# Performance work log

Measured on AMD Instinct MI355X. Metric: run time of the kernel, lower is better.

The kernel has to match this reference:

```python
import jax, jax.numpy as jnp
import numpy as np

DT = 0.01
NJ = 7  # panda: 7 revolute joints, serial chain, fixed base
G_ACC = 9.81


def skew(v):
    x, y, z = v[..., 0], v[..., 1], v[..., 2]
    O = jnp.zeros_like(x)
    return jnp.stack([jnp.stack([O, -z, y], -1),
                      jnp.stack([z, O, -x], -1),
                      jnp.stack([-y, x, O], -1)], -2)


def rodrigues(axis, q):
    # axis [3], q [B] -> [B,3,3]
    K = skew(axis)
    K2 = K @ K
    s = jnp.sin(q)[:, None, None]
    c = jnp.cos(q)[:, None, None]
    return jnp.eye(3, dtype=q.dtype) + s * K + (1.0 - c) * K2


def xmot(E, r, v):
    # motion transform child<-parent; E [B,3,3], r [3], v [B,6] ([w;u] ordering)
    w, u = v[:, :3], v[:, 3:]
    wn = jnp.einsum('bij,bj->bi', E, w)
    un = jnp.einsum('bij,bj->bi', E, u - jnp.cross(jnp.broadcast_to(r, u.shape), w))
    return jnp.concatenate([wn, un], -1)


def crm(v, m):
    # motion cross product v x m
    w, u = v[:, :3], v[:, 3:]
    return jnp.concatenate([jnp.cross(w, m[:, :3]),
                            jnp.cross(w, m[:, 3:]) + jnp.cross(u, m[:, :3])], -1)


def crf(v, f):
    # force cross product v x* f
    w, u = v[:, :3], v[:, 3:]
    n, ff = f[:, :3], f[:, 3:]
    return jnp.concatenate([jnp.cross(w, n) + jnp.cross(u, ff), jnp.cross(w, ff)], -1)


def spatial_inertia(mass, com, inertia):
    # [NJ] / [NJ,3] / [NJ,3,3] -> [NJ,6,6] in [w;v] ordering
    cx = skew(com)
    m = mass[:, None, None]
    top = jnp.concatenate([inertia + m * (cx @ jnp.swapaxes(cx, -1, -2)), m * cx], -1)
    bot = jnp.concatenate([m * jnp.swapaxes(cx, -1, -2),
                           m * jnp.broadcast_to(jnp.eye(3, dtype=mass.dtype), cx.shape)], -1)
    return jnp.concatenate([top, bot], -2)


def aba(q, qd, tau, axes, R_fix, p_fix, mass, com, inertia):
    B = q.shape[0]
    I6 = spatial_inertia(mass, com, inertia)  # [NJ,6,6]
    E_l, S_l, v_l, c_l, IA_l, pA_l = [], [], [], [], [], []
    v_prev = None
    # pass 1: kinematics + bias terms
    for i in range(NJ):
        Rw = jnp.einsum('ij,bjk->bik', R_fix[i], rodrigues(axes[i], q[:, i]))
        E = jnp.swapaxes(Rw, -1, -2)  # parent->child rotation
        S = jnp.concatenate([axes[i], jnp.zeros(3, dtype=q.dtype)])  # [6]
        vJ = qd[:, i:i + 1] * S
        v_i = vJ if i == 0 else xmot(E, p_fix[i], v_prev) + vJ
        c_i = crm(v_i, vJ)
        Iv = jnp.einsum('ij,bj->bi', I6[i], v_i)
        pA_i = crf(v_i, Iv)
        E_l.append(E); S_l.append(S); v_l.append(v_i); c_l.append(c_i)
        IA_l.append(jnp.broadcast_to(I6[i], (B, 6, 6)))
        pA_l.append(pA_i)
        v_prev = v_i
    # pass 2: articulated inertia backward sweep
    U_l = [None] * NJ; d_l = [None] * NJ; uu_l = [None] * NJ
    for i in reversed(range(NJ)):
        S = S_l[i]; IA = IA_l[i]
        U = jnp.einsum('bij,j->bi', IA, S)
        d = jnp.einsum('bi,i->b', U, S)
        uu = tau[:, i] - jnp.einsum('bi,i->b', pA_l[i], S)
        U_l[i], d_l[i], uu_l[i] = U, d, uu
        if i > 0:
            Ia = IA - U[:, :, None] * U[:, None, :] / d[:, None, None]
            pa = pA_l[i] + jnp.einsum('bij,bj->bi', Ia, c_l[i]) + U * (uu / d)[:, None]
            E = E_l[i]; rX = skew(p_fix[i])
            Z = jnp.zeros_like(E)
            Xm = jnp.concatenate([jnp.concatenate([E, Z], -1),
                                  jnp.concatenate([-jnp.einsum('bij,jk->bik', E, rX), E], -1)], -2)
            IA_l[i - 1] = IA_l[i - 1] + jnp.einsum('bji,bjk,bkl->bil', Xm, Ia, Xm)
            fE = jnp.einsum('bji,bj->bi', E, pa[:, 3:])
            nP = jnp.einsum('bji,bj->bi', E, pa[:, :3]) + jnp.cross(jnp.broadcast_to(p_fix[i], fE.shape), fE)
            pA_l[i - 1] = pA_l[i - 1] + jnp.concatenate([nP, fE], -1)
    # pass 3: accelerations (base spatial accel = -gravity)
    a_prev = jnp.broadcast_to(jnp.array([0, 0, 0, 0, 0, G_ACC], dtype=q.dtype), (B, 6))
    qdd = []
    for i in range(NJ):
        ap = xmot(E_l[i], p_fix[i], a_prev) + c_l[i]
        qdd_i = (uu_l[i] - jnp.einsum('bi,bi->b', U_l[i], ap)) / d_l[i]
        a_prev = ap + qdd_i[:, None] * S_l[i]
        qdd.append(qdd_i)
    return jnp.stack(qdd, -1)  # [B,NJ]


def _rx(a):
    c, s = np.cos(a), np.sin(a)
    return np.array([[1, 0, 0], [0, c, -s], [0, s, c]], np.float32)


def setup_inputs() -> dict:
    key = jax.random.key(0)
    k1, k2 = jax.random.split(key)
    B = 262144
    x = 0.5 * jax.random.normal(k1, (B, 2 * NJ), dtype=jnp.float32)
    u = 5.0 * jax.random.normal(k2, (B, NJ), dtype=jnp.float32)
    angles = [0.0, -np.pi / 2, np.pi / 2, np.pi / 2, -np.pi / 2, np.pi / 2, np.pi / 2]
    R_fix = jnp.asarray(np.stack([_rx(a) for a in angles]).astype(np.float32))
    p_fix = jnp.asarray(np.array([[0, 0, 0.333], [0, 0, 0], [0, -0.316, 0], [0.0825, 0, 0],
                                  [-0.0825, 0.384, 0], [0, 0, 0], [0.088, 0, 0]], np.float32))
    axes = jnp.asarray(np.tile(np.array([0, 0, 1], np.float32), (NJ, 1)))
    mass = jnp.asarray(np.array([4.97, 0.65, 3.23, 3.59, 1.23, 1.67, 0.735], np.float32))
    com = jnp.asarray(np.array([[0.003, 0.002, -0.06], [-0.003, -0.028, 0.003], [0.027, 0.039, -0.066],
                                [-0.053, 0.104, 0.027], [-0.012, 0.041, -0.038], [0.06, -0.014, -0.011],
                                [0.01, -0.004, 0.061]], np.float32))
    diags = np.array([[0.7, 0.7, 0.01], [0.008, 0.028, 0.025], [0.037, 0.036, 0.011],
                      [0.026, 0.028, 0.031], [0.036, 0.036, 0.011], [0.002, 0.004, 0.005],
                      [0.012, 0.010, 0.005]], np.float32)
    inertia = jnp.asarray(np.stack([np.diag(v) for v in diags]).astype(np.float32))
    return {"x": x, "u": u, "axes": axes, "R_fix": R_fix, "p_fix": p_fix,
            "mass": mass, "com": com, "inertia": inertia}


def reference(x, u, axes, R_fix, p_fix, mass, com, inertia):
    q, v = x[:, :NJ], x[:, NJ:]
    a = aba(q, v, u, axes, R_fix, p_fix, mass, com, inertia)
    v_next = v + DT * a            # semi-implicit Euler
    q_next = q + DT * v_next
    return jnp.concatenate([q_next, v_next], -1)
```

## Files before the change

### kernel.cpp

```cpp
#include <hip/hip_runtime.h>

#define NJ 7
static constexpr float DT_C    = 0.01f;
static constexpr float G_ACC_C = 9.81f;

static constexpr float RF[NJ][9] = {
    {1,0,0,  0,1,0,  0,0,1},
    {1,0,0,  0,0,1,  0,-1,0},
    {1,0,0,  0,0,-1, 0,1,0},
    {1,0,0,  0,0,-1, 0,1,0},
    {1,0,0,  0,0,1,  0,-1,0},
    {1,0,0,  0,0,-1, 0,1,0},
    {1,0,0,  0,0,-1, 0,1,0},
};
static constexpr float PFX[NJ][3] = {
    {0.f, 0.f, 0.333f},
    {0.f, 0.f, 0.f},
    {0.f, -0.316f, 0.f},
    {0.0825f, 0.f, 0.f},
    {-0.0825f, 0.384f, 0.f},
    {0.f, 0.f, 0.f},
    {0.088f, 0.f, 0.f},
};
static constexpr float MS[NJ] = {4.97f, 0.65f, 3.23f, 3.59f, 1.23f, 1.67f, 0.735f};
static constexpr float CM[NJ][3] = {
    {0.003f, 0.002f, -0.06f},
    {-0.003f, -0.028f, 0.003f},
    {0.027f, 0.039f, -0.066f},
    {-0.053f, 0.104f, 0.027f},
    {-0.012f, 0.041f, -0.038f},
    {0.06f, -0.014f, -0.011f},
    {0.01f, -0.004f, 0.061f},
};
static constexpr float ID[NJ][3] = {
    {0.7f, 0.7f, 0.01f},
    {0.008f, 0.028f, 0.025f},
    {0.037f, 0.036f, 0.011f},
    {0.026f, 0.028f, 0.031f},
    {0.036f, 0.036f, 0.011f},
    {0.002f, 0.004f, 0.005f},
    {0.012f, 0.01f, 0.005f},
};

#define MAKE_E(Rf, s, c)                                                     \
    float E00 = (Rf)[0]*(c) + (Rf)[1]*(s);                                   \
    float E01 = (Rf)[3]*(c) + (Rf)[4]*(s);                                   \
    float E02 = (Rf)[6]*(c) + (Rf)[7]*(s);                                   \
    float E10 = (Rf)[1]*(c) - (Rf)[0]*(s);                                   \
    float E11 = (Rf)[4]*(c) - (Rf)[3]*(s);                                   \
    float E12 = (Rf)[7]*(c) - (Rf)[6]*(s);                                   \
    float E20 = (Rf)[2];                                                     \
    float E21 = (Rf)[5];                                                     \
    float E22 = (Rf)[8];

extern "C" __global__ __launch_bounds__(256)
void aba_step_kernel(const float* __restrict__ x, const float* __restrict__ u,
                     float* __restrict__ out, int B)
{
    int b = blockIdx.x * blockDim.x + threadIdx.x;
    if (b >= B) return;
    const int xb = b * (2*NJ);

    float cl0[NJ], cl1[NJ], cl3[NJ], cl4[NJ];
    float pA[NJ][6];

    {
        float v0=0.f, v1=0.f, v2=0.f, v3=0.f, v4=0.f, v5=0.f;
        #pragma unroll
        for (int i = 0; i < NJ; ++i) {
            float qi = x[xb + i];
            float qd = x[xb + NJ + i];
            float s, c;
            __sincosf(qi, &s, &c);
            MAKE_E(RF[i], s, c)
            if (i == 0) {
                v0 = 0.f; v1 = 0.f; v2 = qd; v3 = 0.f; v4 = 0.f; v5 = 0.f;
            } else {
                const float px = PFX[i][0], py = PFX[i][1], pz = PFX[i][2];
                float t0 = v3 - (py*v2 - pz*v1);
                float t1 = v4 - (pz*v0 - px*v2);
                float t2 = v5 - (px*v1 - py*v0);
                float nw0 = E00*v0 + E01*v1 + E02*v2;
                float nw1 = E10*v0 + E11*v1 + E12*v2;
                float nw2 = E20*v0 + E21*v1 + E22*v2;
                float nu0 = E00*t0 + E01*t1 + E02*t2;
                float nu1 = E10*t0 + E11*t1 + E12*t2;
                float nu2 = E20*t0 + E21*t1 + E22*t2;
                v0 = nw0; v1 = nw1; v2 = nw2 + qd;
                v3 = nu0; v4 = nu1; v5 = nu2;
            }
            cl0[i] =  v1*qd;
            cl1[i] = -v0*qd;
            cl3[i] =  v4*qd;
            cl4[i] = -v3*qd;
            const float m  = MS[i];
            const float cx = CM[i][0], cy = CM[i][1], cz = CM[i][2];
            const float cc = cx*cx + cy*cy + cz*cz;
            const float A0 = ID[i][0] + m*(cc - cx*cx);
            const float A1 = -(m*cx*cy);
            const float A2 = -(m*cx*cz);
            const float A3 = ID[i][1] + m*(cc - cy*cy);
            const float A4 = -(m*cy*cz);
            const float A5 = ID[i][2] + m*(cc - cz*cz);
            float n0 = A0*v0 + A1*v1 + A2*v2 + m*(cy*v5 - cz*v4);
            float n1 = A1*v0 + A3*v1 + A4*v2 + m*(cz*v3 - cx*v5);
            float n2 = A2*v0 + A4*v1 + A5*v2 + m*(cx*v4 - cy*v3);
            float f0 = m*(v1*cz - v2*cy + v3);
            float f1 = m*(v2*cx - v0*cz + v4);
            float f2 = m*(v0*cy - v1*cx + v5);
            pA[i][0] = v1*n2 - v2*n1 + v4*f2 - v5*f1;
            pA[i][1] = v2*n0 - v0*n2 + v5*f0 - v3*f2;
            pA[i][2] = v0*n1 - v1*n0 + v3*f1 - v4*f0;
            pA[i][3] = v1*f2 - v2*f1;
            pA[i][4] = v2*f0 - v0*f2;
            pA[i][5] = v0*f1 - v1*f0;
        }
    }

    float PA[6] = {0,0,0,0,0,0};
    float PB[9] = {0,0,0,0,0,0,0,0,0};
    float PC[6] = {0,0,0,0,0,0};

    #pragma unroll
    for (int ii = 0; ii < NJ; ++ii) {
        const int i = NJ - 1 - ii;
        const float m  = MS[i];
        const float cx = CM[i][0], cy = CM[i][1], cz = CM[i][2];
        const float cc = cx*cx + cy*cy + cz*cz;
        float A0 = ID[i][0] + m*(cc - cx*cx) + PA[0];
        float A1 = -(m*cx*cy)               + PA[1];
        float A2 = -(m*cx*cz)               + PA[2];
        float A3 = ID[i][1] + m*(cc - cy*cy) + PA[3];
        float A4 = -(m*cy*cz)               + PA[4];
        float A5 = ID[i][2] + m*(cc - cz*cz) + PA[5];
        float B00 = PB[0];          float B01 = PB[1] - m*cz;  float B02 = PB[2] + m*cy;
        float B10 = PB[3] + m*cz;   float B11 = PB[4];         float B12 = PB[5] - m*cx;
        float B20 = PB[6] - m*cy;   float B21 = PB[7] + m*cx;  float B22 = PB[8];
        float C0 = PC[0] + m, C1 = PC[1],     C2 = PC[2];
        float C3 = PC[3] + m, C4 = PC[4],     C5 = PC[5] + m;

        float uu   = u[b*NJ + i] - pA[i][2];
        float invd = __builtin_amdgcn_rcpf(A5);
        float k    = uu * invd;
        float t0 = A2*invd, t1 = A4*invd;
        float t3 = B20*invd, t4 = B21*invd, t5 = B22*invd;

        if (i > 0) {
            float a00 = A0 - A2*t0, a01 = A1 - A2*t1, a11 = A3 - A4*t1;
            float b00 = B00 - A2*t3, b01 = B01 - A2*t4, b02 = B02 - A2*t5;
            float b10 = B10 - A4*t3, b11 = B11 - A4*t4, b12 = B12 - A4*t5;
            float c00 = C0 - B20*t3, c01 = C1 - B20*t4, c02 = C2 - B20*t5;
            float c11 = C3 - B21*t4, c12 = C4 - B21*t5, c22 = C5 - B22*t5;

            float q0 = cl0[i], q1 = cl1[i], q3 = cl3[i], q4 = cl4[i];
            float pa0 = pA[i][0] + a00*q0 + a01*q1 + b00*q3 + b01*q4 + A2*k;
            float pa1 = pA[i][1] + a01*q0 + a11*q1 + b10*q3 + b11*q4 + A4*k;
            float pa2 = pA[i][2] + uu;
            float pa3 = pA[i][3] + b00*q0 + b10*q1 + c00*q3 + c01*q4 + B20*k;
            float pa4 = pA[i][4] + b01*q0 + b11*q1 + c01*q3 + c11*q4 + B21*k;
            float pa5 = pA[i][5] + b02*q0 + b12*q1 + c02*q3 + c12*q4 + B22*k;

            float s, c;
            __sincosf(x[xb + i], &s, &c);
            MAKE_E(RF[i], s, c)
            const float px = PFX[i][0], py = PFX[i][1], pz = PFX[i][2];

            float AE00 = a00*E00 + a01*E10, AE01 = a00*E01 + a01*E11, AE02 = a00*E02 + a01*E12;
            float AE10 = a01*E00 + a11*E10, AE11 = a01*E01 + a11*E11, AE12 = a01*E02 + a11*E12;
            float Ap00 = E00*AE00 + E10*AE10;
            float Ap01 = E00*AE01 + E10*AE11;
            float Ap02 = E00*AE02 + E10*AE12;
            float Ap11 = E01*AE01 + E11*AE11;
            float Ap12 = E01*AE02 + E11*AE12;
            float Ap22 = E02*AE02 + E12*AE12;
            float BE00 = b00*E00 + b01*E10 + b02*E20;
            float BE01 = b00*E01 + b01*E11 + b02*E21;
            float BE02 = b00*E02 + b01*E12 + b02*E22;
            float BE10 = b10*E00 + b11*E10 + b12*E20;
            float BE11 = b10*E01 + b11*E11 + b12*E21;
            float BE12 = b10*E02 + b11*E12 + b12*E22;
            float Bp00 = E00*BE00 + E10*BE10, Bp01 = E00*BE01 + E10*BE11, Bp02 = E00*BE02 + E10*BE12;
            float Bp10 = E01*BE00 + E11*BE10, Bp11 = E01*BE01 + E11*BE11, Bp12 = E01*BE02 + E11*BE12;
            float Bp20 = E02*BE00 + E12*BE10, Bp21 = E02*BE01 + E12*BE11, Bp22 = E02*BE02 + E12*BE12;
            float CE00 = c00*E00 + c01*E10 + c02*E20;
            float CE01 = c00*E01 + c01*E11 + c02*E21;
            float CE02 = c00*E02 + c01*E12 + c02*E22;
            float CE10 = c01*E00 + c11*E10 + c12*E20;
            float CE11 = c01*E01 + c11*E11 + c12*E21;
            float CE12 = c01*E02 + c11*E12 + c12*E22;
            float CE20 = c02*E00 + c12*E10 + c22*E20;
            float CE21 = c02*E01 + c12*E11 + c22*E21;
            float CE22 = c02*E02 + c12*E12 + c22*E22;
            float Cp00 = E00*CE00 + E10*CE10 + E20*CE20;
            float Cp01 = E00*CE01 + E10*CE11 + E20*CE21;
            float Cp02 = E00*CE02 + E10*CE12 + E20*CE22;
            float Cp11 = E01*CE01 + E11*CE11 + E21*CE21;
            float Cp12 = E01*CE02 + E11*CE12 + E21*CE22;
            float Cp22 = E02*CE02 + E12*CE12 + E22*CE22;
            float G00 = Bp01*pz - Bp02*py, G01 = Bp02*px - Bp00*pz, G02 = Bp00*py - Bp01*px;
            float G10 = Bp11*pz - Bp12*py, G11 = Bp12*px - Bp10*pz, G12 = Bp10*py - Bp11*px;
            float G20 = Bp21*pz - Bp22*py, G21 = Bp22*px - Bp20*pz, G22 = Bp20*py - Bp21*px;
            float H00 = Cp01*pz - Cp02*py, H01 = Cp02*px - Cp00*pz, H02 = Cp00*py - Cp01*px;
            float H10 = Cp11*pz - Cp12*py, H11 = Cp12*px - Cp01*pz, H12 = Cp01*py - Cp11*px;
            float H20 = Cp12*pz - Cp22*py, H21 = Cp22*px - Cp02*pz, H22 = Cp02*py - Cp12*px;
            float PH00 = py*H20 - pz*H10;
            float PH01 = py*H21 - pz*H11;
            float PH02 = py*H22 - pz*H12;
            float PH11 = pz*H01 - px*H21;
            float PH12 = pz*H02 - px*H22;
            float PH22 = px*H12 - py*H02;
            PA[0] = Ap00 - G00 - G00 - PH00;
            PA[1] = Ap01 - G01 - G10 - PH01;
            PA[2] = Ap02 - G02 - G20 - PH02;
            PA[3] = Ap11 - G11 - G11 - PH11;
            PA[4] = Ap12 - G12 - G21 - PH12;
            PA[5] = Ap22 - G22 - G22 - PH22;
            PB[0] = Bp00 + py*Cp02 - pz*Cp01;
            PB[1] = Bp01 + py*Cp12 - pz*Cp11;
            PB[2] = Bp02 + py*Cp22 - pz*Cp12;
            PB[3] = Bp10 + pz*Cp00 - px*Cp02;
            PB[4] = Bp11 + pz*Cp01 - px*Cp12;
            PB[5] = Bp12 + pz*Cp02 - px*Cp22;
            PB[6] = Bp20 + px*Cp01 - py*Cp00;
            PB[7] = Bp21 + px*Cp11 - py*Cp01;
            PB[8] = Bp22 + px*Cp12 - py*Cp02;
            PC[0] = Cp00; PC[1] = Cp01; PC[2] = Cp02;
            PC[3] = Cp11; PC[4] = Cp12; PC[5] = Cp22;
            float fE0 = E00*pa3 + E10*pa4 + E20*pa5;
            float fE1 = E01*pa3 + E11*pa4 + E21*pa5;
            float fE2 = E02*pa3 + E12*pa4 + E22*pa5;
            float nP0 = E00*pa0 + E10*pa1 + E20*pa2 + (py*fE2 - pz*fE1);
            float nP1 = E01*pa0 + E11*pa1 + E21*pa2 + (pz*fE0 - px*fE2);
            float nP2 = E02*pa0 + E12*pa1 + E22*pa2 + (px*fE1 - py*fE0);
            pA[i-1][0] += nP0; pA[i-1][1] += nP1; pA[i-1][2] += nP2;
            pA[i-1][3] += fE0; pA[i-1][4] += fE1; pA[i-1][5] += fE2;
        }
        pA[i][0] = t0; pA[i][1] = t1; pA[i][2] = t3;
        pA[i][3] = t4; pA[i][4] = t5; pA[i][5] = k;
    }

    {
        float a0=0.f, a1=0.f, a2=0.f, a3=0.f, a4=0.f, a5=G_ACC_C;
        #pragma unroll
        for (int i = 0; i < NJ; ++i) {
            float qi = x[xb + i];
            float qd = x[xb + NJ + i];
            float s, c;
            __sincosf(qi, &s, &c);
            MAKE_E(RF[i], s, c)
            const float px = PFX[i][0], py = PFX[i][1], pz = PFX[i][2];
            float t0 = a3 - (py*a2 - pz*a1);
            float t1 = a4 - (pz*a0 - px*a2);
            float t2 = a5 - (px*a1 - py*a0);
            float ap0 = E00*a0 + E01*a1 + E02*a2 + cl0[i];
            float ap1 = E10*a0 + E11*a1 + E12*a2 + cl1[i];
            float ap2 = E20*a0 + E21*a1 + E22*a2;
            float ap3 = E00*t0 + E01*t1 + E02*t2 + cl3[i];
            float ap4 = E10*t0 + E11*t1 + E12*t2 + cl4[i];
            float ap5 = E20*t0 + E21*t1 + E22*t2;
            float qdd = pA[i][5] - (pA[i][0]*ap0 + pA[i][1]*ap1 + ap2
                                  + pA[i][2]*ap3 + pA[i][3]*ap4 + pA[i][4]*ap5);
            a0 = ap0; a1 = ap1; a2 = ap2 + qdd;
            a3 = ap3; a4 = ap4; a5 = ap5;
            float vn = qd + DT_C*qdd;
            out[xb + NJ + i] = vn;
            out[xb + i]      = qi + DT_C*vn;
        }
    }
}

extern "C" void kernel_launch(void* const* d_in, const int* in_sizes, int n_in,
                              void* d_out, int out_size, void* d_ws, size_t ws_size,
                              hipStream_t stream) {
    const float* x = (const float*)d_in[0];
    const float* u = (const float*)d_in[1];
    float* out = (float*)d_out;
    int B = in_sizes[0] / (2*NJ);
    int threads = 256;
    int blocks = (B + threads - 1) / threads;
    hipLaunchKernelGGL(aba_step_kernel, dim3(blocks), dim3(threads), 0, stream,
                       x, u, out, B);
}
```

Before: 107.2 us.

## Stage inputs and outputs through LDS with coalesced float4 transfers, cache sincos

Each block now loads its slab of x and u into shared memory with coalesced float4 loads, computes from LDS, and writes results back through a shared buffer with float4 stores. Previously each thread read its own strided 14-float row, which coalesces poorly. The sin/cos values computed in the first pass are kept in LDS and reused, so the later passes no longer call sincos. The cost is about 37 KB of LDS per block and two barriers, which may lower occupancy.

```diff
diff --git a/kernel.cpp b/kernel.cpp
--- a/kernel.cpp
+++ b/kernel.cpp
@@ -1,6 +1,7 @@
 #include <hip/hip_runtime.h>
 
 #define NJ 7
+#define TB 256
 static constexpr float DT_C    = 0.01f;
 static constexpr float G_ACC_C = 9.81f;
 
@@ -57,215 +58,262 @@
 void aba_step_kernel(const float* __restrict__ x, const float* __restrict__ u,
                      float* __restrict__ out, int B)
 {
-    int b = blockIdx.x * blockDim.x + threadIdx.x;
-    if (b >= B) return;
-    const int xb = b * (2*NJ);
-
-    float cl0[NJ], cl1[NJ], cl3[NJ], cl4[NJ];
-    float pA[NJ][6];
-
-    {
-        float v0=0.f, v1=0.f, v2=0.f, v3=0.f, v4=0.f, v5=0.f;
+    __shared__ float xbuf [TB * 14];
+    __shared__ float ubuf [TB * 7];
+    __shared__ float scbuf[TB * 14];
+
+    const int tid = threadIdx.x;
+    const int b0  = blockIdx.x * TB;
+    const int nb  = min(TB, B - b0);
+
+    if (nb == TB) {
+        const float4* xv = (const float4*)(x + b0 * 14);
+        float4*       xl = (float4*)xbuf;
         #pragma unroll
-        for (int i = 0; i < NJ; ++i) {
-            float qi = x[xb + i];
-            float qd = x[xb + NJ + i];
-            float s, c;
-            __sincosf(qi, &s, &c);
-            MAKE_E(RF[i], s, c)
-            if (i == 0) {
-                v0 = 0.f; v1 = 0.f; v2 = qd; v3 = 0.f; v4 = 0.f; v5 = 0.f;
-            } else {
-                const float px = PFX[i][0], py = PFX[i][1], pz = PFX[i][2];
-                float t0 = v3 - (py*v2 - pz*v1);
-                float t1 = v4 - (pz*v0 - px*v2);
-                float t2 = v5 - (px*v1 - py*v0);
-                float nw0 = E00*v0 + E01*v1 + E02*v2;
-                float nw1 = E10*v0 + E11*v1 + E12*v2;
-                float nw2 = E20*v0 + E21*v1 + E22*v2;
-                float nu0 = E00*t0 + E01*t1 + E02*t2;
-                float nu1 = E10*t0 + E11*t1 + E12*t2;
-                float nu2 = E20*t0 + E21*t1 + E22*t2;
-                v0 = nw0; v1 = nw1; v2 = nw2 + qd;
-                v3 = nu0; v4 = nu1; v5 = nu2;
+        for (int k = 0; k < 4; ++k) {
+            int idx = tid + k * TB;
+            if (idx < 896) xl[idx] = xv[idx];
+        }
+        const float4* uv = (const float4*)(u + b0 * 7);
+        float4*       ul = (float4*)ubuf;
+        #pragma unroll
+        for (int k = 0; k < 2; ++k) {
+            int idx = tid + k * TB;
+            if (idx < 448) ul[idx] = uv[idx];
+        }
+    } else {
+        int nx = nb * 14;
+        for (int t = tid; t < nx; t += TB) xbuf[t] = x[b0 * 14 + t];
+        int nu = nb * 7;
+        for (int t = tid; t < nu; t += TB) ubuf[t] = u[b0 * 7 + t];
+    }
+    __syncthreads();
+
+    if (tid < nb) {
+        const float* xr  = xbuf  + tid * 14;
+        const float* ur  = ubuf  + tid * 7;
+        float*       scr = scbuf + tid * 14;
+
+        float cl0[NJ], cl1[NJ], cl3[NJ], cl4[NJ];
+        float pA[NJ][6];
+
+        {
+            float v0=0.f, v1=0.f, v2=0.f, v3=0.f, v4=0.f, v5=0.f;
+            #pragma unroll
+            for (int i = 0; i < NJ; ++i) {
+                float qi = xr[i];
+                float qd = xr[7 + i];
+                float s, c;
+                __sincosf(qi, &s, &c);
+                scr[i]     = s;
+                scr[7 + i] = c;
+                MAKE_E(RF[i], s, c)
+                if (i == 0) {
+                    v0 = 0.f; v1 = 0.f; v2 = qd; v3 = 0.f; v4 = 0.f; v5 = 0.f;
+                } else {
+                    const float px = PFX[i][0], py = PFX[i][1], pz = PFX[i][2];
+                    float t0 = v3 - (py*v2 - pz*v1);
+                    float t1 = v4 - (pz*v0 - px*v2);
+                    float t2 = v5 - (px*v1 - py*v0);
+                    float nw0 = E00*v0 + E01*v1 + E02*v2;
+                    float nw1 = E10*v0 + E11*v1 + E12*v2;
+                    float nw2 = E20*v0 + E21*v1 + E22*v2;
+                    float nu0 = E00*t0 + E01*t1 + E02*t2;
+                    float nu1 = E10*t0 + E11*t1 + E12*t2;
+                    float nu2 = E20*t0 + E21*t1 + E22*t2;
+                    v0 = nw0; v1 = nw1; v2 = nw2 + qd;
+                    v3 = nu0; v4 = nu1; v5 = nu2;
+                }
+                cl0[i] =  v1*qd;
+                cl1[i] = -v0*qd;
+                cl3[i] =  v4*qd;
+                cl4[i] = -v3*qd;
+                const float m  = MS[i];
+                const float cx = CM[i][0], cy = CM[i][1], cz = CM[i][2];
+                const float cc = cx*cx + cy*cy + cz*cz;
+                const float A0 = ID[i][0] + m*(cc - cx*cx);
+                const float A1 = -(m*cx*cy);
+                const float A2 = -(m*cx*cz);
+                const float A3 = ID[i][1] + m*(cc - cy*cy);
+                const float A4 = -(m*cy*cz);
+                const float A5 = ID[i][2] + m*(cc - cz*cz);
+                float n0 = A0*v0 + A1*v1 + A2*v2 + m*(cy*v5 - cz*v4);
+                float n1 = A1*v0 + A3*v1 + A4*v2 + m*(cz*v3 - cx*v5);
+                float n2 = A2*v0 + A4*v1 + A5*v2 + m*(cx*v4 - cy*v3);
+                float f0 = m*(v1*cz - v2*cy + v3);
+                float f1 = m*(v2*cx - v0*cz + v4);
+                float f2 = m*(v0*cy - v1*cx + v5);
+                pA[i][0] = v1*n2 - v2*n1 + v4*f2 - v5*f1;
+                pA[i][1] = v2*n0 - v0*n2 + v5*f0 - v3*f2;
+                pA[i][2] = v0*n1 - v1*n0 + v3*f1 - v4*f0;
+                pA[i][3] = v1*f2 - v2*f1;
+                pA[i][4] = v2*f0 - v0*f2;
+                pA[i][5] = v0*f1 - v1*f0;
             }
-            cl0[i] =  v1*qd;
-            cl1[i] = -v0*qd;
-            cl3[i] =  v4*qd;
-            cl4[i] = -v3*qd;
+        }
+
+        float PA[6] = {0,0,0,0,0,0};
+        float PB[9] = {0,0,0,0,0,0,0,0,0};
+        float PC[6] = {0,0,0,0,0,0};
+
+        #pragma unroll
+        for (int ii = 0; ii < NJ; ++ii) {
+            const int i = NJ - 1 - ii;
             const float m  = MS[i];
             const float cx = CM[i][0], cy = CM[i][1], cz = CM[i][2];
             const float cc = cx*cx + cy*cy + cz*cz;
-            const float A0 = ID[i][0] + m*(cc - cx*cx);
-            const float A1 = -(m*cx*cy);
-            const float A2 = -(m*cx*cz);
-            const float A3 = ID[i][1] + m*(cc - cy*cy);
-            const float A4 = -(m*cy*cz);
-            const float A5 = ID[i][2] + m*(cc - cz*cz);
-            float n0 = A0*v0 + A1*v1 + A2*v2 + m*(cy*v5 - cz*v4);
-            float n1 = A1*v0 + A3*v1 + A4*v2 + m*(cz*v3 - cx*v5);
-            float n2 = A2*v0 + A4*v1 + A5*v2 + m*(cx*v4 - cy*v3);
-            float f0 = m*(v1*cz - v2*cy + v3);
-            float f1 = m*(v2*cx - v0*cz + v4);
-            float f2 = m*(v0*cy - v1*cx + v5);
-            pA[i][0] = v1*n2 - v2*n1 + v4*f2 - v5*f1;
-            pA[i][1] = v2*n0 - v0*n2 + v5*f0 - v3*f2;
-            pA[i][2] = v0*n1 - v1*n0 + v3*f1 - v4*f0;
-            pA[i][3] = v1*f2 - v2*f1;
-            pA[i][4] = v2*f0 - v0*f2;
-            pA[i][5] = v0*f1 - v1*f0;
+            float A0 = ID[i][0] + m*(cc - cx*cx) + PA[0];
+            float A1 = -(m*cx*cy)               + PA[1];
+            float A2 = -(m*cx*cz)               + PA[2];
+            float A3 = ID[i][1] + m*(cc - cy*cy) + PA[3];
+            float A4 = -(m*cy*cz)               + PA[4];
+            float A5 = ID[i][2] + m*(cc - cz*cz) + PA[5];
+            float B00 = PB[0];          float B01 = PB[1] - m*cz;  float B02 = PB[2] + m*cy;
+            float B10 = PB[3] + m*cz;   float B11 = PB[4];         float B12 = PB[5] - m*cx;
+            float B20 = PB[6] - m*cy;   float B21 = PB[7] + m*cx;  float B22 = PB[8];
+            float C0 = PC[0] + m, C1 = PC[1],     C2 = PC[2];
+            float C3 = PC[3] + m, C4 = PC[4],     C5 = PC[5] + m;
+
+            float uu   = ur[i] - pA[i][2];
+            float invd = __builtin_amdgcn_rcpf(A5);
+            float k    = uu * invd;
+            float t0 = A2*invd, t1 = A4*invd;
+            float t3 = B20*invd, t4 = B21*invd, t5 = B22*invd;
+
+            if (i > 0) {
+                float a00 = A0 - A2*t0, a01 = A1 - A2*t1, a11 = A3 - A4*t1;
+                float b00 = B00 - A2*t3, b01 = B01 - A2*t4, b02 = B02 - A2*t5;
+                float b10 = B10 - A4*t3, b11 = B11 - A4*t4, b12 = B12 - A4*t5;
+                float c00 = C0 - B20*t3, c01 = C1 - B20*t4, c02 = C2 - B20*t5;
+                float c11 = C3 - B21*t4, c12 = C4 - B21*t5, c22 = C5 - B22*t5;
+
+                float q0 = cl0[i], q1 = cl1[i], q3 = cl3[i], q4 = cl4[i];
+                float pa0 = pA[i][0] + a00*q0 + a01*q1 + b00*q3 + b01*q4 + A2*k;
+                float pa1 = pA[i][1] + a01*q0 + a11*q1 + b10*q3 + b11*q4 + A4*k;
+                float pa2 = pA[i][2] + uu;
+                float pa3 = pA[i][3] + b00*q0 + b10*q1 + c00*q3 + c01*q4 + B20*k;
+                float pa4 = pA[i][4] + b01*q0 + b11*q1 + c01*q3 + c11*q4 + B21*k;
+                float pa5 = pA[i][5] + b02*q0 + b12*q1 + c02*q3 + c12*q4 + B22*k;
+
+                float s = scr[i], c = scr[7 + i];
+                MAKE_E(RF[i], s, c)
+                const float px = PFX[i][0], py = PFX[i][1], pz = PFX[i][2];
+
+                float AE00 = a00*E00 + a01*E10, AE01 = a00*E01 + a01*E11, AE02 = a00*E02 + a01*E12;
+                float AE10 = a01*E00 + a11*E10, AE11 = a01*E01 + a11*E11, AE12 = a01*E02 + a11*E12;
+                float Ap00 = E00*AE00 + E10*AE10;
+                float Ap01 = E00*AE01 + E10*AE11;
+                float Ap02 = E00*AE02 + E10*AE12;
+                float Ap11 = E01*AE01 + E11*AE11;
+                float Ap12 = E01*AE02 + E11*AE12;
+                float Ap22 = E02*AE02 + E12*AE12;
+                float BE00 = b00*E00 + b01*E10 + b02*E20;
+                float BE01 = b00*E01 + b01*E11 + b02*E21;
+                float BE02 = b00*E02 + b01*E12 + b02*E22;
+                float BE10 = b10*E00 + b11*E10 + b12*E20;
+                float BE11 = b10*E01 + b11*E11 + b12*E21;
+                float BE12 = b10*E02 + b11*E12 + b12*E22;
+                float Bp00 = E00*BE00 + E10*BE10, Bp01 = E00*BE01 + E10*BE11, Bp02 = E00*BE02 + E10*BE12;
+                float Bp10 = E01*BE00 + E11*BE10, Bp11 = E01*BE01 + E11*BE11, Bp12 = E01*BE02 + E11*BE12;
+                float Bp20 = E02*BE00 + E12*BE10, Bp21 = E02*BE01 + E12*BE11, Bp22 = E02*BE02 + E12*BE12;
+                float CE00 = c00*E00 + c01*E10 + c02*E20;
+                float CE01 = c00*E01 + c01*E11 + c02*E21;
+                float CE02 = c00*E02 + c01*E12 + c02*E22;
+                float CE10 = c01*E00 + c11*E10 + c12*E20;
+                float CE11 = c01*E01 + c11*E11 + c12*E21;
+                float CE12 = c01*E02 + c11*E12 + c12*E22;
+                float CE20 = c02*E00 + c12*E10 + c22*E20;
+                float CE21 = c02*E01 + c12*E11 + c22*E21;
+                float CE22 = c02*E02 + c12*E12 + c22*E22;
+                float Cp00 = E00*CE00 + E10*CE10 + E20*CE20;
+                float Cp01 = E00*CE01 + E10*CE11 + E20*CE21;
+                float Cp02 = E00*CE02 + E10*CE12 + E20*CE22;
+                float Cp11 = E01*CE01 + E11*CE11 + E21*CE21;
+                float Cp12 = E01*CE02 + E11*CE12 + E21*CE22;
+                float Cp22 = E02*CE02 + E12*CE12 + E22*CE22;
+                float G00 = Bp01*pz - Bp02*py, G01 = Bp02*px - Bp00*pz, G02 = Bp00*py - Bp01*px;
+                float G10 = Bp11*pz - Bp12*py, G11 = Bp12*px - Bp10*pz, G12 = Bp10*py - Bp11*px;
+                float G20 = Bp21*pz - Bp22*py, G21 = Bp22*px - Bp20*pz, G22 = Bp20*py - Bp21*px;
+                float H00 = Cp01*pz - Cp02*py, H01 = Cp02*px - Cp00*pz, H02 = Cp00*py - Cp01*px;
+                float H10 = Cp11*pz - Cp12*py, H11 = Cp12*px - Cp01*pz, H12 = Cp01*py - Cp11*px;
+                float H20 = Cp12*pz - Cp22*py, H21 = Cp22*px - Cp02*pz, H22 = Cp02*py - Cp12*px;
+                float PH00 = py*H20 - pz*H10;
+                float PH01 = py*H21 - pz*H11;
+                float PH02 = py*H22 - pz*H12;
+                float PH11 = pz*H01 - px*H21;
+                float PH12 = pz*H02 - px*H22;
+                float PH22 = px*H12 - py*H02;
+                PA[0] = Ap00 - G00 - G00 - PH00;
+                PA[1] = Ap01 - G01 - G10 - PH01;
+                PA[2] = Ap02 - G02 - G20 - PH02;
+                PA[3] = Ap11 - G11 - G11 - PH11;
+                PA[4] = Ap12 - G12 - G21 - PH12;
+                PA[5] = Ap22 - G22 - G22 - PH22;
+                PB[0] = Bp00 + py*Cp02 - pz*Cp01;
+                PB[1] = Bp01 + py*Cp12 - pz*Cp11;
+                PB[2] = Bp02 + py*Cp22 - pz*Cp12;
+                PB[3] = Bp10 + pz*Cp00 - px*Cp02;
+                PB[4] = Bp11 + pz*Cp01 - px*Cp12;
+                PB[5] = Bp12 + pz*Cp02 - px*Cp22;
+                PB[6] = Bp20 + px*Cp01 - py*Cp00;
+                PB[7] = Bp21 + px*Cp11 - py*Cp01;
+                PB[8] = Bp22 + px*Cp12 - py*Cp02;
+                PC[0] = Cp00; PC[1] = Cp01; PC[2] = Cp02;
+                PC[3] = Cp11; PC[4] = Cp12; PC[5] = Cp22;
+                float fE0 = E00*pa3 + E10*pa4 + E20*pa5;
+                float fE1 = E01*pa3 + E11*pa4 + E21*pa5;
+                float fE2 = E02*pa3 + E12*pa4 + E22*pa5;
+                float nP0 = E00*pa0 + E10*pa1 + E20*pa2 + (py*fE2 - pz*fE1);
+                float nP1 = E01*pa0 + E11*pa1 + E21*pa2 + (pz*fE0 - px*fE2);
+                float nP2 = E02*pa0 + E12*pa1 + E22*pa2 + (px*fE1 - py*fE0);
+                pA[i-1][0] += nP0; pA[i-1][1] += nP1; pA[i-1][2] += nP2;
+                pA[i-1][3] += fE0; pA[i-1][4] += fE1; pA[i-1][5] += fE2;
+            }
+            pA[i][0] = t0; pA[i][1] = t1; pA[i][2] = t3;
+            pA[i][3] = t4; pA[i][4] = t5; pA[i][5] = k;
+        }
+
+        {
+            float a0=0.f, a1=0.f, a2=0.f, a3=0.f, a4=0.f, a5=G_ACC_C;
+            #pragma unroll
+            for (int i = 0; i < NJ; ++i) {
+                float qi = xr[i];
+                float qd = xr[7 + i];
+                float s = scr[i], c = scr[7 + i];
+                MAKE_E(RF[i], s, c)
+                const float px = PFX[i][0], py = PFX[i][1], pz = PFX[i][2];
+                float t0 = a3 - (py*a2 - pz*a1);
+                float t1 = a4 - (pz*a0 - px*a2);
+                float t2 = a5 - (px*a1 - py*a0);
+                float ap0 = E00*a0 + E01*a1 + E02*a2 + cl0[i];
+                float ap1 = E10*a0 + E11*a1 + E12*a2 + cl1[i];
+                float ap2 = E20*a0 + E21*a1 + E22*a2;
+                float ap3 = E00*t0 + E01*t1 + E02*t2 + cl3[i];
+                float ap4 = E10*t0 + E11*t1 + E12*t2 + cl4[i];
+                float ap5 = E20*t0 + E21*t1 + E22*t2;
+                float qdd = pA[i][5] - (pA[i][0]*ap0 + pA[i][1]*ap1 + ap2
+                                      + pA[i][2]*ap3 + pA[i][3]*ap4 + pA[i][4]*ap5);
+                a0 = ap0; a1 = ap1; a2 = ap2 + qdd;
+                a3 = ap3; a4 = ap4; a5 = ap5;
+                float vn = qd + DT_C*qdd;
+                scr[7 + i] = vn;
+                scr[i]     = qi + DT_C*vn;
+            }
         }
     }
 
-    float PA[6] = {0,0,0,0,0,0};
-    float PB[9] = {0,0,0,0,0,0,0,0,0};
-    float PC[6] = {0,0,0,0,0,0};
-
-    #pragma unroll
-    for (int ii = 0; ii < NJ; ++ii) {
-        const int i = NJ - 1 - ii;
-        const float m  = MS[i];
-        const float cx = CM[i][0], cy = CM[i][1], cz = CM[i][2];
-        const float cc = cx*cx + cy*cy + cz*cz;
-        float A0 = ID[i][0] + m*(cc - cx*cx) + PA[0];
-        float A1 = -(m*cx*cy)               + PA[1];
-        float A2 = -(m*cx*cz)               + PA[2];
-        float A3 = ID[i][1] + m*(cc - cy*cy) + PA[3];
-        float A4 = -(m*cy*cz)               + PA[4];
-        float A5 = ID[i][2] + m*(cc - cz*cz) + PA[5];
-        float B00 = PB[0];          float B01 = PB[1] - m*cz;  float B02 = PB[2] + m*cy;
-        float B10 = PB[3] + m*cz;   float B11 = PB[4];         float B12 = PB[5] - m*cx;
-        float B20 = PB[6] - m*cy;   float B21 = PB[7] + m*cx;  float B22 = PB[8];
-        float C0 = PC[0] + m, C1 = PC[1],     C2 = PC[2];
-        float C3 = PC[3] + m, C4 = PC[4],     C5 = PC[5] + m;
-
-        float uu   = u[b*NJ + i] - pA[i][2];
-        float invd = __builtin_amdgcn_rcpf(A5);
-        float k    = uu * invd;
-        float t0 = A2*invd, t1 = A4*invd;
-        float t3 = B20*invd, t4 = B21*invd, t5 = B22*invd;
-
-        if (i > 0) {
-            float a00 = A0 - A2*t0, a01 = A1 - A2*t1, a11 = A3 - A4*t1;
-            float b00 = B00 - A2*t3, b01 = B01 - A2*t4, b02 = B02 - A2*t5;
-            float b10 = B10 - A4*t3, b11 = B11 - A4*t4, b12 = B12 - A4*t5;
-            float c00 = C0 - B20*t3, c01 = C1 - B20*t4, c02 = C2 - B20*t5;
-            float c11 = C3 - B21*t4, c12 = C4 - B21*t5, c22 = C5 - B22*t5;
-
-            float q0 = cl0[i], q1 = cl1[i], q3 = cl3[i], q4 = cl4[i];
-            float pa0 = pA[i][0] + a00*q0 + a01*q1 + b00*q3 + b01*q4 + A2*k;
-            float pa1 = pA[i][1] + a01*q0 + a11*q1 + b10*q3 + b11*q4 + A4*k;
-            float pa2 = pA[i][2] + uu;
-            float pa3 = pA[i][3] + b00*q0 + b10*q1 + c00*q3 + c01*q4 + B20*k;
-            float pa4 = pA[i][4] + b01*q0 + b11*q1 + c01*q3 + c11*q4 + B21*k;
-            float pa5 = pA[i][5] + b02*q0 + b12*q1 + c02*q3 + c12*q4 + B22*k;
-
-            float s, c;
-            __sincosf(x[xb + i], &s, &c);
-            MAKE_E(RF[i], s, c)
-            const float px = PFX[i][0], py = PFX[i][1], pz = PFX[i][2];
-
-            float AE00 = a00*E00 + a01*E10, AE01 = a00*E01 + a01*E11, AE02 = a00*E02 + a01*E12;
-            float AE10 = a01*E00 + a11*E10, AE11 = a01*E01 + a11*E11, AE12 = a01*E02 + a11*E12;
-            float Ap00 = E00*AE00 + E10*AE10;
-            float Ap01 = E00*AE01 + E10*AE11;
-            float Ap02 = E00*AE02 + E10*AE12;
-            float Ap11 = E01*AE01 + E11*AE11;
-            float Ap12 = E01*AE02 + E11*AE12;
-            float Ap22 = E02*AE02 + E12*AE12;
-            float BE00 = b00*E00 + b01*E10 + b02*E20;
-            float BE01 = b00*E01 + b01*E11 + b02*E21;
-            float BE02 = b00*E02 + b01*E12 + b02*E22;
-            float BE10 = b10*E00 + b11*E10 + b12*E20;
-            float BE11 = b10*E01 + b11*E11 + b12*E21;
-            float BE12 = b10*E02 + b11*E12 + b12*E22;
-            float Bp00 = E00*BE00 + E10*BE10, Bp01 = E00*BE01 + E10*BE11, Bp02 = E00*BE02 + E10*BE12;
-            float Bp10 = E01*BE00 + E11*BE10, Bp11 = E01*BE01 + E11*BE11, Bp12 = E01*BE02 + E11*BE12;
-            float Bp20 = E02*BE00 + E12*BE10, Bp21 = E02*BE01 + E12*BE11, Bp22 = E02*BE02 + E12*BE12;
-            float CE00 = c00*E00 + c01*E10 + c02*E20;
-            float CE01 = c00*E01 + c01*E11 + c02*E21;
-            float CE02 = c00*E02 + c01*E12 + c02*E22;
-            float CE10 = c01*E00 + c11*E10 + c12*E20;
-            float CE11 = c01*E01 + c11*E11 + c12*E21;
-            float CE12 = c01*E02 + c11*E12 + c12*E22;
-            float CE20 = c02*E00 + c12*E10 + c22*E20;
-            float CE21 = c02*E01 + c12*E11 + c22*E21;
-            float CE22 = c02*E02 + c12*E12 + c22*E22;
-            float Cp00 = E00*CE00 + E10*CE10 + E20*CE20;
-            float Cp01 = E00*CE01 + E10*CE11 + E20*CE21;
-            float Cp02 = E00*CE02 + E10*CE12 + E20*CE22;
-            float Cp11 = E01*CE01 + E11*CE11 + E21*CE21;
-            float Cp12 = E01*CE02 + E11*CE12 + E21*CE22;
-            float Cp22 = E02*CE02 + E12*CE12 + E22*CE22;
-            float G00 = Bp01*pz - Bp02*py, G01 = Bp02*px - Bp00*pz, G02 = Bp00*py - Bp01*px;
-            float G10 = Bp11*pz - Bp12*py, G11 = Bp12*px - Bp10*pz, G12 = Bp10*py - Bp11*px;
-            float G20 = Bp21*pz - Bp22*py, G21 = Bp22*px - Bp20*pz, G22 = Bp20*py - Bp21*px;
-            float H00 = Cp01*pz - Cp02*py, H01 = Cp02*px - Cp00*pz, H02 = Cp00*py - Cp01*px;
-            float H10 = Cp11*pz - Cp12*py, H11 = Cp12*px - Cp01*pz, H12 = Cp01*py - Cp11*px;
-            float H20 = Cp12*pz - Cp22*py, H21 = Cp22*px - Cp02*pz, H22 = Cp02*py - Cp12*px;
-            float PH00 = py*H20 - pz*H10;
-            float PH01 = py*H21 - pz*H11;
-            float PH02 = py*H22 - pz*H12;
-            float PH11 = pz*H01 - px*H21;
-            float PH12 = pz*H02 - px*H22;
-            float PH22 = px*H12 - py*H02;
-            PA[0] = Ap00 - G00 - G00 - PH00;
-            PA[1] = Ap01 - G01 - G10 - PH01;
-            PA[2] = Ap02 - G02 - G20 - PH02;
-            PA[3] = Ap11 - G11 - G11 - PH11;
-            PA[4] = Ap12 - G12 - G21 - PH12;
-            PA[5] = Ap22 - G22 - G22 - PH22;
-            PB[0] = Bp00 + py*Cp02 - pz*Cp01;
-            PB[1] = Bp01 + py*Cp12 - pz*Cp11;
-            PB[2] = Bp02 + py*Cp22 - pz*Cp12;
-            PB[3] = Bp10 + pz*Cp00 - px*Cp02;
-            PB[4] = Bp11 + pz*Cp01 - px*Cp12;
-            PB[5] = Bp12 + pz*Cp02 - px*Cp22;
-            PB[6] = Bp20 + px*Cp01 - py*Cp00;
-            PB[7] = Bp21 + px*Cp11 - py*Cp01;
-            PB[8] = Bp22 + px*Cp12 - py*Cp02;
-            PC[0] = Cp00; PC[1] = Cp01; PC[2] = Cp02;
-            PC[3] = Cp11; PC[4] = Cp12; PC[5] = Cp22;
-            float fE0 = E00*pa3 + E10*pa4 + E20*pa5;
-            float fE1 = E01*pa3 + E11*pa4 + E21*pa5;
-            float fE2 = E02*pa3 + E12*pa4 + E22*pa5;
-            float nP0 = E00*pa0 + E10*pa1 + E20*pa2 + (py*fE2 - pz*fE1);
-            float nP1 = E01*pa0 + E11*pa1 + E21*pa2 + (pz*fE0 - px*fE2);
-            float nP2 = E02*pa0 + E12*pa1 + E22*pa2 + (px*fE1 - py*fE0);
-            pA[i-1][0] += nP0; pA[i-1][1] += nP1; pA[i-1][2] += nP2;
-            pA[i-1][3] += fE0; pA[i-1][4] += fE1; pA[i-1][5] += fE2;
-        }
-        pA[i][0] = t0; pA[i][1] = t1; pA[i][2] = t3;
-        pA[i][3] = t4; pA[i][4] = t5; pA[i][5] = k;
-    }
-
-    {
-        float a0=0.f, a1=0.f, a2=0.f, a3=0.f, a4=0.f, a5=G_ACC_C;
+    __syncthreads();
+    if (nb == TB) {
+        float4*       ov = (float4*)(out + b0 * 14);
+        const float4* sl = (const float4*)scbuf;
         #pragma unroll
-        for (int i = 0; i < NJ; ++i) {
-            float qi = x[xb + i];
-            float qd = x[xb + NJ + i];
-            float s, c;
-            __sincosf(qi, &s, &c);
-            MAKE_E(RF[i], s, c)
-            const float px = PFX[i][0], py = PFX[i][1], pz = PFX[i][2];
-            float t0 = a3 - (py*a2 - pz*a1);
-            float t1 = a4 - (pz*a0 - px*a2);
-            float t2 = a5 - (px*a1 - py*a0);
-            float ap0 = E00*a0 + E01*a1 + E02*a2 + cl0[i];
-            float ap1 = E10*a0 + E11*a1 + E12*a2 + cl1[i];
-            float ap2 = E20*a0 + E21*a1 + E22*a2;
-            float ap3 = E00*t0 + E01*t1 + E02*t2 + cl3[i];
-            float ap4 = E10*t0 + E11*t1 + E12*t2 + cl4[i];
-            float ap5 = E20*t0 + E21*t1 + E22*t2;
-            float qdd = pA[i][5] - (pA[i][0]*ap0 + pA[i][1]*ap1 + ap2
-                                  + pA[i][2]*ap3 + pA[i][3]*ap4 + pA[i][4]*ap5);
-            a0 = ap0; a1 = ap1; a2 = ap2 + qdd;
-            a3 = ap3; a4 = ap4; a5 = ap5;
-            float vn = qd + DT_C*qdd;
-            out[xb + NJ + i] = vn;
-            out[xb + i]      = qi + DT_C*vn;
-        }
+        for (int k = 0; k < 4; ++k) {
+            int idx = tid + k * TB;
+            if (idx < 896) ov[idx] = sl[idx];
+        }
+    } else {
+        int nx = nb * 14;
+        for (int t = tid; t < nx; t += TB) out[b0 * 14 + t] = scbuf[t];
     }
 }
 
@@ -276,7 +324,7 @@
     const float* u = (const float*)d_in[1];
     float* out = (float*)d_out;
     int B = in_sizes[0] / (2*NJ);
-    int threads = 256;
+    int threads = TB;
     int blocks = (B + threads - 1) / threads;
     hipLaunchKernelGGL(aba_step_kernel, dim3(blocks), dim3(threads), 0, stream,
                        x, u, out, B);
```

New measurement: 105.9 us. About the same (-1.2%).
